# Optimization experiments

Hardware: AMD Instinct MI355X
Metric: run time of the kernel (lower is better)

## Reference

```python
import jax, jax.numpy as jnp
import numpy as np

BATCH, SEQ, D_IN, UNITS = 32, 2048, 256, 256


def setup_inputs() -> dict:
    key = jax.random.key(0)
    k1, k2, k3 = jax.random.split(key, 3)
    x = jax.random.normal(k1, (BATCH, SEQ, D_IN), dtype=jnp.float32)
    # packed gate weights in order [i, f, g, o]
    W = jax.random.normal(k2, (D_IN, 4 * UNITS), dtype=jnp.float32) * (1.0 / np.sqrt(D_IN))
    U = jax.random.normal(k3, (UNITS, 4 * UNITS), dtype=jnp.float32) * (1.0 / np.sqrt(UNITS))
    b = jnp.zeros((4 * UNITS,), dtype=jnp.float32)
    return {"x": x, "W": W, "U": U, "b": b}


def reference(x, W, U, b):
    """LSTM layer: zero init states, loop over time, return all hidden states.
    x: [B, T, D]; W: [D, 4H]; U: [H, 4H]; b: [4H] -> out: [B, T, H]."""
    B = x.shape[0]
    H = U.shape[0]
    # Precompute the input contribution for all timesteps in one big GEMM.
    xW = jnp.einsum('btd,dg->btg', x, W) + b  # [B, T, 4H]

    def step(carry, xw_t):
        h, c = carry
        gates = xw_t + h @ U  # [B, 4H]
        i, f, g, o = jnp.split(gates, 4, axis=-1)
        i = jax.nn.sigmoid(i)
        f = jax.nn.sigmoid(f)
        g = jnp.tanh(g)
        o = jax.nn.sigmoid(o)
        c = f * c + i * g
        h = o * jnp.tanh(c)
        return (h, c), h

    h0 = jnp.zeros((B, H), dtype=x.dtype)
    c0 = jnp.zeros((B, H), dtype=x.dtype)
    # scan over time: xW transposed to [T, B, 4H]
    _, hs = jax.lax.scan(step, (h0, c0), jnp.swapaxes(xW, 0, 1))
    return jnp.swapaxes(hs, 0, 1)  # [B, T, H]
```

## Files before the change

### kernel.cpp

```cpp
#include <hip/hip_runtime.h>
#include <hip/hip_fp16.h>

typedef _Float16 f16;
typedef _Float16 f16x2 __attribute__((ext_vector_type(2)));
typedef _Float16 f16x8 __attribute__((ext_vector_type(8)));
typedef float f32x4 __attribute__((ext_vector_type(4)));
typedef unsigned int u32;

#define BATCH 32
#define SEQT  2048
#define DIN   256
#define HU    256
#define G4    1024
#define MROWS (BATCH*SEQT)

#define WS_XW 0
#define WS_XH 134217728UL
#define WS_WT 167772160UL
#define WS_UP 168296448UL
#define WS_NEED 168820736UL

__global__ void pack_u(const float* __restrict__ U, u32* __restrict__ upk) {
    int idx = blockIdx.x * 256 + threadIdx.x;
    int p = idx >> 10, j = idx & 1023;
    f16x2 h;
    h.x = (f16)U[(2 * p) * G4 + j];
    h.y = (f16)U[(2 * p + 1) * G4 + j];
    upk[p * G4 + j] = __builtin_bit_cast(u32, h);
}

__global__ void conv_x(const float* __restrict__ x, f16* __restrict__ xh) {
    int idx = blockIdx.x * 256 + threadIdx.x;
    int row = idx >> 5, c = idx & 31;
    const float4* src = (const float4*)(x + row * 256 + c * 8);
    float4 v0 = src[0], v1 = src[1];
    f16x8 o;
    o[0] = (f16)v0.x; o[1] = (f16)v0.y; o[2] = (f16)v0.z; o[3] = (f16)v0.w;
    o[4] = (f16)v1.x; o[5] = (f16)v1.y; o[6] = (f16)v1.z; o[7] = (f16)v1.w;
    *(f16x8*)(xh + row * 256 + c * 8) = o;
}

__global__ void conv_w(const float* __restrict__ W, f16* __restrict__ wt) {
    int idx = blockIdx.x * 256 + threadIdx.x;
    int j = idx >> 5, c = idx & 31;
    f16x8 o;
#pragma unroll
    for (int i = 0; i < 8; ++i) o[i] = (f16)W[(c * 8 + i) * G4 + j];
    *(f16x8*)(wt + j * 256 + c * 8) = o;
}

__launch_bounds__(256)
__global__ void gemm_xw(const f16* __restrict__ xh, const f16* __restrict__ wt,
                        const float* __restrict__ bias, f16* __restrict__ xw) {
    __shared__ __align__(16) f16 As[128 * 256];
    __shared__ __align__(16) f16 Bs[128 * 256];
    int mt = blockIdx.x, nt = blockIdx.y;
    int t = threadIdx.x, lane = t & 63, w = t >> 6;

    const uint4* Ag = (const uint4*)(xh + (size_t)mt * 128 * 256);
    const uint4* Bg = (const uint4*)(wt + (size_t)nt * 128 * 256);
#pragma unroll
    for (int i = 0; i < 16; ++i) {
        int o16 = t + i * 256;
        int row = o16 >> 5, c = o16 & 31;
        uint4 va = Ag[o16];
        uint4 vb = Bg[o16];
        int sw = c ^ (row & 7);
        *(uint4*)((char*)As + row * 512 + sw * 16) = va;
        *(uint4*)((char*)Bs + row * 512 + sw * 16) = vb;
    }
    __syncthreads();

    int wr = w >> 1, wc = w & 1;
    f32x4 acc[4][4];
#pragma unroll
    for (int mi = 0; mi < 4; ++mi)
#pragma unroll
        for (int ni = 0; ni < 4; ++ni) acc[mi][ni] = (f32x4){0.f, 0.f, 0.f, 0.f};

    int rA = lane & 15;
    int kg = lane >> 4;
#pragma unroll
    for (int ks = 0; ks < 8; ++ks) {
        f16x8 af[4], bf[4];
#pragma unroll
        for (int mi = 0; mi < 4; ++mi) {
            int row = wr * 64 + mi * 16 + rA;
            int c = ks * 4 + kg;
            af[mi] = *(const f16x8*)((const char*)As + row * 512 + ((c ^ (row & 7)) * 16));
        }
#pragma unroll
        for (int ni = 0; ni < 4; ++ni) {
            int row = wc * 64 + ni * 16 + rA;
            int c = ks * 4 + kg;
            bf[ni] = *(const f16x8*)((const char*)Bs + row * 512 + ((c ^ (row & 7)) * 16));
        }
#pragma unroll
        for (int mi = 0; mi < 4; ++mi)
#pragma unroll
            for (int ni = 0; ni < 4; ++ni)
                acc[mi][ni] = __builtin_amdgcn_mfma_f32_16x16x32_f16(af[mi], bf[ni], acc[mi][ni], 0, 0, 0);
    }

    int r4 = (lane >> 4) * 4, cc = lane & 15;
    float bv[4];
#pragma unroll
    for (int ni = 0; ni < 4; ++ni) bv[ni] = bias[nt * 128 + wc * 64 + ni * 16 + cc];
#pragma unroll
    for (int mi = 0; mi < 4; ++mi)
#pragma unroll
        for (int ni = 0; ni < 4; ++ni)
#pragma unroll
            for (int q = 0; q < 4; ++q) {
                int grow = mt * 128 + wr * 64 + mi * 16 + r4 + q;
                int gcol = nt * 128 + wc * 64 + ni * 16 + cc;
                xw[(size_t)grow * 1024 + gcol] = (f16)(acc[mi][ni][q] + bv[ni]);
            }
}

__device__ __forceinline__ float fdot2u(u32 u, u32 h, float acc) {
    return __builtin_amdgcn_fdot2(__builtin_bit_cast(f16x2, u),
                                  __builtin_bit_cast(f16x2, h), acc, false);
}
__device__ __forceinline__ float sigm(float x) {
    return 1.0f / (1.0f + __expf(-x));
}
__device__ __forceinline__ float tanh_f(float x) {
    x = fminf(fmaxf(x, -15.0f), 15.0f);
    float e = __expf(2.0f * x);
    return (e - 1.0f) / (e + 1.0f);
}


#define DECLC(c) uint4 uc_##c;
#define LOADC(c) do {                              \
    uc_##c.x = upk[(4*(c)+0)*1024 + t];            \
    uc_##c.y = upk[(4*(c)+1)*1024 + t];            \
    uc_##c.z = upk[(4*(c)+2)*1024 + t];            \
    uc_##c.w = upk[(4*(c)+3)*1024 + t];            \
} while (0)
#define CHR(c) do {                                \
    uint4 hv = *(const uint4*)&hpair[4*(c)];       \
    a0 = fdot2u(uc_##c.x, hv.x, a0);               \
    a1 = fdot2u(uc_##c.y, hv.y, a1);               \
    a2 = fdot2u(uc_##c.z, hv.z, a2);               \
    a3 = fdot2u(uc_##c.w, hv.w, a3);               \
} while (0)

__launch_bounds__(1024)
__global__ void lstm_rec(const u32* __restrict__ upk, const f16* __restrict__ xw,
                         float* __restrict__ out) {
    __shared__ __align__(16) u32 ulds[1024 * 36];
    __shared__ __align__(16) u32 hpair[128];
    __shared__ __align__(16) float gbuf[1024];

    int b = blockIdx.x, t = threadIdx.x;

    DECLC(0)  DECLC(1)  DECLC(2)  DECLC(3)  DECLC(4)  DECLC(5)
    DECLC(6)  DECLC(7)  DECLC(8)  DECLC(9)  DECLC(10) DECLC(11)
    DECLC(12) DECLC(13) DECLC(14) DECLC(15) DECLC(16) DECLC(17)
    DECLC(18) DECLC(19) DECLC(20) DECLC(21) DECLC(22)

    LOADC(0);  LOADC(1);  LOADC(2);  LOADC(3);  LOADC(4);  LOADC(5);
    LOADC(6);  LOADC(7);  LOADC(8);  LOADC(9);  LOADC(10); LOADC(11);
    LOADC(12); LOADC(13); LOADC(14); LOADC(15); LOADC(16); LOADC(17);
    LOADC(18); LOADC(19); LOADC(20); LOADC(21); LOADC(22);

#pragma unroll
    for (int i = 0; i < 36; ++i)
        ulds[t * 36 + i] = upk[(92 + i) * 1024 + t];
    if (t < 128) hpair[t] = 0u;

    float c_state = 0.0f;
    const f16* xp = xw + (size_t)b * SEQT * G4;
    float* op = out + (size_t)b * SEQT * HU;
    f16 xa = xp[t];
    __syncthreads();

    for (int st = 0; st < SEQT; ++st) {
        float a0 = (float)xa, a1 = 0.f, a2 = 0.f, a3 = 0.f;
        if (st < SEQT - 1) xa = xp[G4 + t];
        xp += G4;

        CHR(0);  CHR(1);  CHR(2);  CHR(3);  CHR(4);  CHR(5);
        CHR(6);  CHR(7);  CHR(8);  CHR(9);  CHR(10); CHR(11);
        CHR(12); CHR(13); CHR(14); CHR(15); CHR(16); CHR(17);
        CHR(18); CHR(19); CHR(20); CHR(21); CHR(22);

#pragma unroll
        for (int ch = 0; ch < 9; ++ch) {
            uint4 hv = *(const uint4*)&hpair[92 + ch * 4];
            uint4 u4 = *(const uint4*)&ulds[t * 36 + ch * 4];
            a0 = fdot2u(u4.x, hv.x, a0);
            a1 = fdot2u(u4.y, hv.y, a1);
            a2 = fdot2u(u4.z, hv.z, a2);
            a3 = fdot2u(u4.w, hv.w, a3);
        }
        float a = (a0 + a1) + (a2 + a3);

        float act = ((t >> 8) == 2) ? tanh_f(a) : sigm(a);
        gbuf[t] = act;
        __syncthreads();

        if (t < 256) {
            float gi = gbuf[t];
            float gf = gbuf[256 + t];
            float gg = gbuf[512 + t];
            float go = gbuf[768 + t];
            c_state = gf * c_state + gi * gg;
            float h = go * tanh_f(c_state);
            op[t] = h;
            ((f16*)hpair)[t] = (f16)h;
        }
        op += HU;
        __syncthreads();
    }
}

extern "C" void kernel_launch(void* const* d_in, const int* in_sizes, int n_in,
                              void* d_out, int out_size, void* d_ws, size_t ws_size,
                              hipStream_t stream) {
    const float* x    = (const float*)d_in[0];
    const float* W    = (const float*)d_in[1];
    const float* U    = (const float*)d_in[2];
    const float* bias = (const float*)d_in[3];
    float* out = (float*)d_out;

    if (ws_size < WS_NEED) return;
    char* ws = (char*)d_ws;
    f16* xw  = (f16*)(ws + WS_XW);
    f16* xh  = (f16*)(ws + WS_XH);
    f16* wt  = (f16*)(ws + WS_WT);
    u32* upk = (u32*)(ws + WS_UP);

    pack_u<<<512, 256, 0, stream>>>(U, upk);
    conv_x<<<8192, 256, 0, stream>>>(x, xh);
    conv_w<<<128, 256, 0, stream>>>(W, wt);
    gemm_xw<<<dim3(512, 8), 256, 0, stream>>>(xh, wt, bias, xw);
    lstm_rec<<<32, 1024, 0, stream>>>(upk, xw, out);
}
```

Baseline: 4.135 ms.

## Split each batch's LSTM recurrence across two workgroups with global-memory h exchange

Each batch row's recurrence now runs on two 512-thread workgroups, each owning half of the hidden units and the matching gate columns. Every step they swap their half of h through global memory, guarded by acquire/release flags and spin-waiting. Each workgroup first computes the dot products against its own half of h, then waits for the partner's half, which hides part of the exchange latency. The aim is to double the CUs in use and halve per-step work per workgroup, at the cost of a cross-CU handshake on every timestep and a bounded spin that could silently read stale data if it times out.

Measured after the change: 5.235 ms. 1.27x slower.

```diff
diff --git a/kernel.cpp b/kernel.cpp
--- a/kernel.cpp
+++ b/kernel.cpp
@@ -18,7 +18,9 @@
 #define WS_XH 134217728UL
 #define WS_WT 167772160UL
 #define WS_UP 168296448UL
-#define WS_NEED 168820736UL
+#define WS_HX 168820736UL
+#define WS_FLG 168837120UL
+#define WS_NEED 168841216UL
 
 __global__ void pack_u(const float* __restrict__ U, u32* __restrict__ upk) {
     int idx = blockIdx.x * 256 + threadIdx.x;
@@ -133,63 +135,94 @@
 
 
 #define DECLC(c) uint4 uc_##c;
-#define LOADC(c) do {                              \
-    uc_##c.x = upk[(4*(c)+0)*1024 + t];            \
-    uc_##c.y = upk[(4*(c)+1)*1024 + t];            \
-    uc_##c.z = upk[(4*(c)+2)*1024 + t];            \
-    uc_##c.w = upk[(4*(c)+3)*1024 + t];            \
+#define LOADP(c, pb) do {                              \
+    uc_##c.x = upk[((pb)+4*(c)+0)*1024 + col];         \
+    uc_##c.y = upk[((pb)+4*(c)+1)*1024 + col];         \
+    uc_##c.z = upk[((pb)+4*(c)+2)*1024 + col];         \
+    uc_##c.w = upk[((pb)+4*(c)+3)*1024 + col];         \
 } while (0)
-#define CHR(c) do {                                \
-    uint4 hv = *(const uint4*)&hpair[4*(c)];       \
-    a0 = fdot2u(uc_##c.x, hv.x, a0);               \
-    a1 = fdot2u(uc_##c.y, hv.y, a1);               \
-    a2 = fdot2u(uc_##c.z, hv.z, a2);               \
-    a3 = fdot2u(uc_##c.w, hv.w, a3);               \
+#define CHP(c, hb) do {                                \
+    uint4 hv = *(const uint4*)&hpair[(hb) + 4*(c)];    \
+    a0 = fdot2u(uc_##c.x, hv.x, a0);                   \
+    a1 = fdot2u(uc_##c.y, hv.y, a1);                   \
+    a2 = fdot2u(uc_##c.z, hv.z, a2);                   \
+    a3 = fdot2u(uc_##c.w, hv.w, a3);                   \
 } while (0)
 
-__launch_bounds__(1024)
+__launch_bounds__(512)
 __global__ void lstm_rec(const u32* __restrict__ upk, const f16* __restrict__ xw,
-                         float* __restrict__ out) {
-    __shared__ __align__(16) u32 ulds[1024 * 36];
+                         float* __restrict__ out, u32* hx, int* flg) {
+    __shared__ __align__(16) u32 ulds[512 * 36];
     __shared__ __align__(16) u32 hpair[128];
-    __shared__ __align__(16) float gbuf[1024];
-
-    int b = blockIdx.x, t = threadIdx.x;
+    __shared__ __align__(16) float gbuf[512];
+
+    int wg = blockIdx.x, b = wg >> 1, half = wg & 1;
+    int t = threadIdx.x;
+    int col = (t >> 7) * 256 + half * 128 + (t & 127);
+
+    const int pown = half * 64;
+    const int ppart = (1 - half) * 64;
 
     DECLC(0)  DECLC(1)  DECLC(2)  DECLC(3)  DECLC(4)  DECLC(5)
     DECLC(6)  DECLC(7)  DECLC(8)  DECLC(9)  DECLC(10) DECLC(11)
     DECLC(12) DECLC(13) DECLC(14) DECLC(15) DECLC(16) DECLC(17)
     DECLC(18) DECLC(19) DECLC(20) DECLC(21) DECLC(22)
 
-    LOADC(0);  LOADC(1);  LOADC(2);  LOADC(3);  LOADC(4);  LOADC(5);
-    LOADC(6);  LOADC(7);  LOADC(8);  LOADC(9);  LOADC(10); LOADC(11);
-    LOADC(12); LOADC(13); LOADC(14); LOADC(15); LOADC(16); LOADC(17);
-    LOADC(18); LOADC(19); LOADC(20); LOADC(21); LOADC(22);
+    LOADP(0, pown);  LOADP(1, pown);  LOADP(2, pown);  LOADP(3, pown);
+    LOADP(4, pown);  LOADP(5, pown);  LOADP(6, pown);  LOADP(7, pown);
+    LOADP(8, pown);  LOADP(9, pown);  LOADP(10, pown); LOADP(11, pown);
+    LOADP(12, pown); LOADP(13, pown); LOADP(14, pown); LOADP(15, pown);
+    LOADP(16, ppart - 64); LOADP(17, ppart - 64); LOADP(18, ppart - 64);
+    LOADP(19, ppart - 64); LOADP(20, ppart - 64); LOADP(21, ppart - 64);
+    LOADP(22, ppart - 64);
 
 #pragma unroll
     for (int i = 0; i < 36; ++i)
-        ulds[t * 36 + i] = upk[(92 + i) * 1024 + t];
+        ulds[t * 36 + i] = upk[(ppart + 28 + i) * 1024 + col];
     if (t < 128) hpair[t] = 0u;
+
+    u32* hx_own  = hx + (size_t)(b * 2 + half) * 64;
+    u32* hx_part = hx + (size_t)(b * 2 + 1 - half) * 64;
+    int* flg_own  = flg + (b * 2 + half) * 16;
+    int* flg_part = flg + (b * 2 + 1 - half) * 16;
 
     float c_state = 0.0f;
     const f16* xp = xw + (size_t)b * SEQT * G4;
-    float* op = out + (size_t)b * SEQT * HU;
-    f16 xa = xp[t];
+    float* op = out + (size_t)b * SEQT * HU + half * 128;
+    f16 xa = xp[col];
     __syncthreads();
 
     for (int st = 0; st < SEQT; ++st) {
         float a0 = (float)xa, a1 = 0.f, a2 = 0.f, a3 = 0.f;
-        if (st < SEQT - 1) xa = xp[G4 + t];
+        if (st < SEQT - 1) xa = xp[G4 + col];
         xp += G4;
 
-        CHR(0);  CHR(1);  CHR(2);  CHR(3);  CHR(4);  CHR(5);
-        CHR(6);  CHR(7);  CHR(8);  CHR(9);  CHR(10); CHR(11);
-        CHR(12); CHR(13); CHR(14); CHR(15); CHR(16); CHR(17);
-        CHR(18); CHR(19); CHR(20); CHR(21); CHR(22);
-
+        CHP(0, pown);  CHP(1, pown);  CHP(2, pown);  CHP(3, pown);
+        CHP(4, pown);  CHP(5, pown);  CHP(6, pown);  CHP(7, pown);
+        CHP(8, pown);  CHP(9, pown);  CHP(10, pown); CHP(11, pown);
+        CHP(12, pown); CHP(13, pown); CHP(14, pown); CHP(15, pown);
+
+        if (t == 0) {
+            int spins = 0;
+            while (__hip_atomic_load(flg_part, __ATOMIC_ACQUIRE,
+                                     __HIP_MEMORY_SCOPE_AGENT) < st &&
+                   spins < (1 << 22)) {
+                __builtin_amdgcn_s_sleep(2);
+                ++spins;
+            }
+        }
+        __syncthreads();
+        if (t < 64)
+            hpair[ppart + t] = __hip_atomic_load(hx_part + t, __ATOMIC_RELAXED,
+                                                 __HIP_MEMORY_SCOPE_AGENT);
+        __syncthreads();
+
+        CHP(16, ppart - 64); CHP(17, ppart - 64); CHP(18, ppart - 64);
+        CHP(19, ppart - 64); CHP(20, ppart - 64); CHP(21, ppart - 64);
+        CHP(22, ppart - 64);
 #pragma unroll
         for (int ch = 0; ch < 9; ++ch) {
-            uint4 hv = *(const uint4*)&hpair[92 + ch * 4];
+            uint4 hv = *(const uint4*)&hpair[ppart + 28 + ch * 4];
             uint4 u4 = *(const uint4*)&ulds[t * 36 + ch * 4];
             a0 = fdot2u(u4.x, hv.x, a0);
             a1 = fdot2u(u4.y, hv.y, a1);
@@ -198,22 +231,30 @@
         }
         float a = (a0 + a1) + (a2 + a3);
 
-        float act = ((t >> 8) == 2) ? tanh_f(a) : sigm(a);
+        float act = ((t >> 7) == 2) ? tanh_f(a) : sigm(a);
         gbuf[t] = act;
         __syncthreads();
 
-        if (t < 256) {
+        if (t < 128) {
             float gi = gbuf[t];
-            float gf = gbuf[256 + t];
-            float gg = gbuf[512 + t];
-            float go = gbuf[768 + t];
+            float gf = gbuf[128 + t];
+            float gg = gbuf[256 + t];
+            float go = gbuf[384 + t];
             c_state = gf * c_state + gi * gg;
             float h = go * tanh_f(c_state);
             op[t] = h;
-            ((f16*)hpair)[t] = (f16)h;
+            ((f16*)hpair)[half * 128 + t] = (f16)h;
         }
         op += HU;
         __syncthreads();
+
+        if (t < 64)
+            __hip_atomic_store(hx_own + t, hpair[pown + t], __ATOMIC_RELAXED,
+                               __HIP_MEMORY_SCOPE_AGENT);
+        __syncthreads();
+        if (t == 0)
+            __hip_atomic_store(flg_own, st + 1, __ATOMIC_RELEASE,
+                               __HIP_MEMORY_SCOPE_AGENT);
     }
 }
 
@@ -232,10 +273,14 @@
     f16* xh  = (f16*)(ws + WS_XH);
     f16* wt  = (f16*)(ws + WS_WT);
     u32* upk = (u32*)(ws + WS_UP);
+    u32* hx  = (u32*)(ws + WS_HX);
+    int* flg = (int*)(ws + WS_FLG);
+
+    hipMemsetAsync(ws + WS_HX, 0, WS_NEED - WS_HX, stream);
 
     pack_u<<<512, 256, 0, stream>>>(U, upk);
     conv_x<<<8192, 256, 0, stream>>>(x, xh);
     conv_w<<<128, 256, 0, stream>>>(W, wt);
     gemm_xw<<<dim3(512, 8), 256, 0, stream>>>(xh, wt, bias, xw);
-    lstm_rec<<<32, 1024, 0, stream>>>(upk, xw, out);
-}
+    lstm_rec<<<64, 512, 0, stream>>>(upk, xw, out, hx, flg);
+}
```
